# Kernel tuning notes

Measured on AMD Instinct MI355X. Metric: run time of the kernel, lower is better.

The kernel has to match this reference:

```python
import jax, jax.numpy as jnp
import numpy as np

N, E, G = 50000, 500000, 2000   # nodes, edges, graphs
IN, H, ED, OUT = 64, 128, 16, 1
NUM_GAT = 2                      # num_layers - 1
T = 2                            # num_timesteps


def leaky(x, s=0.01):
    return jnp.where(x >= 0, x, s * x)


def gru_cell(x, h, wih, whh, bih, bhh):
    gi = x @ wih.T + bih
    gh = h @ whh.T + bhh
    ir, iz, inn = jnp.split(gi, 3, -1)
    hr, hz, hn = jnp.split(gh, 3, -1)
    r = jax.nn.sigmoid(ir + hr)
    z = jax.nn.sigmoid(iz + hz)
    n = jnp.tanh(inn + r * hn)
    return (1.0 - z) * n + z * h


def lstm_cell(x, h, c, wih, whh, bih, bhh):
    g = x @ wih.T + bih + h @ whh.T + bhh
    i, f, gg, o = jnp.split(g, 4, -1)
    c2 = jax.nn.sigmoid(f) * c + jax.nn.sigmoid(i) * jnp.tanh(gg)
    h2 = jax.nn.sigmoid(o) * jnp.tanh(c2)
    return h2, c2


def setup_inputs() -> dict:
    key = jax.random.key(0)
    ks = iter(jax.random.split(key, 40))
    def rn(shape, s=0.05):
        return jax.random.normal(next(ks), shape, jnp.float32) * s
    return {
        "x": jax.random.normal(next(ks), (N, IN), jnp.float32),
        "edge_index": jax.random.randint(next(ks), (2, E), 0, N),
        "edge_attr": jax.random.normal(next(ks), (E, ED), jnp.float32),
        "batch": jnp.sort(jax.random.randint(next(ks), (N,), 0, G)),
        "lin1_w": rn((H, IN)), "lin1_b": rn((H,)),
        "nd_lin1_w": rn((H, H + ED)), "nd_lin2_w": rn((H, H)), "nd_bias": rn((H,)),
        "gru0_wih": rn((3 * H, H)), "gru0_whh": rn((3 * H, H)),
        "gru0_bih": rn((3 * H,)), "gru0_bhh": rn((3 * H,)),
        "gat_w": rn((NUM_GAT, H, H)), "gat_asrc": rn((NUM_GAT, H)),
        "gat_adst": rn((NUM_GAT, H)), "gat_b": rn((NUM_GAT, H)),
        "gru_wih": rn((NUM_GAT, 3 * H, H)), "gru_whh": rn((NUM_GAT, 3 * H, H)),
        "gru_bih": rn((NUM_GAT, 3 * H)), "gru_bhh": rn((NUM_GAT, 3 * H)),
        "gin_w": rn((H, H)), "gin_b": rn((H,)),
        "lstm_wih": rn((4 * H, H)), "lstm_whh": rn((4 * H, H)),
        "lstm_bih": rn((4 * H,)), "lstm_bhh": rn((4 * H,)),
        "lin2_w": rn((OUT, H)), "lin2_b": rn((OUT,)),
    }


def reference(x, edge_index, edge_attr, batch,
              lin1_w, lin1_b, nd_lin1_w, nd_lin2_w, nd_bias,
              gru0_wih, gru0_whh, gru0_bih, gru0_bhh,
              gat_w, gat_asrc, gat_adst, gat_b,
              gru_wih, gru_whh, gru_bih, gru_bhh,
              gin_w, gin_b, lstm_wih, lstm_whh, lstm_bih, lstm_bhh,
              lin2_w, lin2_b):
    src, dst = edge_index[0], edge_index[1]  # PyG: messages flow src(j) -> dst(i)
    # input projection
    x1 = leaky(x @ lin1_w.T + lin1_b)
    # nd_conv: gather -> MLP -> scatter-add (dropout=0 in eval)
    m = leaky(jnp.concatenate([x1[src], edge_attr], -1) @ nd_lin1_w.T) @ nd_lin2_w.T
    h = jax.nn.elu(jax.ops.segment_sum(m, dst, num_segments=N) + nd_bias)
    xcur = jax.nn.relu(gru_cell(h, x1, gru0_wih, gru0_whh, gru0_bih, gru0_bhh))
    # GAT layers (heads=1, no self loops, negative_slope=0.01)
    for l in range(NUM_GAT):
        xp = xcur @ gat_w[l].T
        a = leaky(xp[src] @ gat_asrc[l] + xp[dst] @ gat_adst[l], 0.01)
        amax = jax.lax.stop_gradient(jax.ops.segment_max(a, dst, num_segments=N))
        ae = jnp.exp(a - amax[dst])
        denom = jax.ops.segment_sum(ae, dst, num_segments=N)
        alpha = ae / denom[dst]
        h = jax.nn.elu(jax.ops.segment_sum(alpha[:, None] * xp[src], dst, num_segments=N) + gat_b[l])
        xcur = jax.nn.relu(gru_cell(h, xcur,
                                    gru_wih[l], gru_whh[l], gru_bih[l], gru_bhh[l]))
    # global readout: GIN on bipartite (nodes -> graphs) + LSTM refinement
    agg = jax.ops.segment_sum(xcur, batch, num_segments=G)  # [G, H], constant over timesteps
    out = jax.nn.relu(agg)
    for _ in range(T):
        h = jax.nn.elu((out + agg) @ gin_w.T + gin_b)  # GIN eps=0: nn(x_dst + aggr)
        out, _ = lstm_cell(out, h, h, lstm_wih, lstm_whh, lstm_bih, lstm_bhh)
    return out @ lin2_w.T + lin2_b  # [G, OUT]
```

## Files before the change

### kernel.cpp

```cpp
#include <hip/hip_runtime.h>
#include <cstdint>
#include <cmath>

#define NN 50000
#define EE 500000
#define GG 2000

#define DEV __device__ __forceinline__

typedef __attribute__((ext_vector_type(8))) short short8;
typedef __attribute__((ext_vector_type(4))) float floatx4;
typedef _Float16 half2v __attribute__((ext_vector_type(2)));
typedef _Float16 half4v __attribute__((ext_vector_type(4)));
typedef _Float16 half8v __attribute__((ext_vector_type(8)));

DEV float fsig(float x) { return 1.f / (1.f + __expf(-x)); }
DEV float ftanh(float x) {
    const float e = __expf(-2.f * fabsf(x));
    const float t = (1.f - e) / (1.f + e);
    return x >= 0.f ? t : -t;
}

DEV float actf(float x, int act) {
    if (act == 1) return x >= 0.f ? x : 0.01f * x;
    if (act == 2) return x > 0.f ? x : __expf(x) - 1.f;
    if (act == 3) return x > 0.f ? x : 0.f;
    return x;
}

DEV float hdot2(half2v a, half2v b, float c) {
#if __has_builtin(__builtin_amdgcn_fdot2)
    return __builtin_amdgcn_fdot2(a, b, c, false);
#else
    return c + (float)a[0] * (float)b[0] + (float)a[1] * (float)b[1];
#endif
}

#define H2(v, i) __builtin_shufflevector(v, v, 2 * (i), 2 * (i) + 1)

__global__ __launch_bounds__(256) void gemm_f16_k(
    const _Float16* __restrict__ A, const _Float16* __restrict__ W,
    const float* __restrict__ bias, _Float16* __restrict__ C,
    int M, int K, int Nout, int act)
{
    __shared__ unsigned short Als[64 * 136];
    __shared__ unsigned short Bls[64 * 136];
    const int tid = threadIdx.x;
    const int bm = blockIdx.y * 64;
    const int bn = blockIdx.x * 64;

    const int ks = (K == 128) ? 7 : 6;
    const int km = K - 1;
    const int nch = (64 * K) >> 3;
    for (int i = tid; i < nch; i += 256) {
        const int e8 = i << 3;
        const int r = e8 >> ks;
        const int c = e8 & km;
        short8 av = {};
        if (bm + r < M) av = *(const short8*)(A + (size_t)(bm + r) * K + c);
        *(short8*)(Als + r * 136 + c) = av;
        *(short8*)(Bls + r * 136 + c) = *(const short8*)(W + (size_t)(bn + r) * K + c);
    }
    __syncthreads();

    const int wave = tid >> 6;
    const int lane = tid & 63;
    const int wr = (wave >> 1) * 32;
    const int wc = (wave & 1) * 32;
    const int l15 = lane & 15;
    const int quad = lane >> 4;

    floatx4 acc00 = {}, acc01 = {}, acc10 = {}, acc11 = {};
    for (int k0 = 0; k0 < K; k0 += 32) {
        const half8v a0 = *(const half8v*)(Als + (wr + l15) * 136 + k0 + quad * 8);
        const half8v a1 = *(const half8v*)(Als + (wr + 16 + l15) * 136 + k0 + quad * 8);
        const half8v b0 = *(const half8v*)(Bls + (wc + l15) * 136 + k0 + quad * 8);
        const half8v b1 = *(const half8v*)(Bls + (wc + 16 + l15) * 136 + k0 + quad * 8);
        acc00 = __builtin_amdgcn_mfma_f32_16x16x32_f16(a0, b0, acc00, 0, 0, 0);
        acc01 = __builtin_amdgcn_mfma_f32_16x16x32_f16(a0, b1, acc01, 0, 0, 0);
        acc10 = __builtin_amdgcn_mfma_f32_16x16x32_f16(a1, b0, acc10, 0, 0, 0);
        acc11 = __builtin_amdgcn_mfma_f32_16x16x32_f16(a1, b1, acc11, 0, 0, 0);
    }

    const floatx4* accs[4] = { &acc00, &acc01, &acc10, &acc11 };
#pragma unroll
    for (int r = 0; r < 2; ++r) {
#pragma unroll
        for (int c = 0; c < 2; ++c) {
            const floatx4 a = *accs[r * 2 + c];
            const int n = bn + wc + c * 16 + l15;
            const float bv = bias ? bias[n] : 0.f;
#pragma unroll
            for (int i = 0; i < 4; ++i) {
                const int m = bm + wr + r * 16 + quad * 4 + i;
                if (m < M) C[(size_t)m * Nout + n] = (_Float16)actf(a[i] + bv, act);
            }
        }
    }
}

__global__ __launch_bounds__(256, 4) void gru_fused4_k(
    const _Float16* __restrict__ xin, const _Float16* __restrict__ hin,
    const _Float16* __restrict__ wih, const _Float16* __restrict__ whh,
    const float* __restrict__ bih, const float* __restrict__ bhh,
    _Float16* __restrict__ xout, int M)
{
    __shared__ unsigned short sX[64 * 136];
    __shared__ unsigned short sH[64 * 136];

    const int tid = threadIdx.x;
    const int bm = blockIdx.x * 64;

    for (int i = tid; i < 1024; i += 256) {
        const int e8 = i << 3;
        const int r = e8 >> 7;
        const int c = e8 & 127;
        const int m = bm + r;
        short8 xv = {}, hv = {};
        if (m < M) {
            xv = *(const short8*)(xin + (size_t)m * 128 + c);
            hv = *(const short8*)(hin + (size_t)m * 128 + c);
        }
        *(short8*)(sX + r * 136 + c) = xv;
        *(short8*)(sH + r * 136 + c) = hv;
    }
    __syncthreads();

    const int wave = tid >> 6;
    const int lane = tid & 63;
    const int l15 = lane & 15;
    const int quad = lane >> 4;
    const int j0 = (blockIdx.y * 4 + wave) * 16;
    const int j = j0 + l15;

    const float br  = bih[j] + bhh[j];
    const float bz  = bih[128 + j] + bhh[128 + j];
    const float bni = bih[256 + j];
    const float bnh = bhh[256 + j];

    floatx4 aR[4] = {}, aZ[4] = {}, aNi[4] = {}, aNh[4] = {};

#pragma unroll
    for (int k = 0; k < 4; ++k) {
        const size_t wrow = (size_t)(j0 + l15) * 128 + k * 32 + quad * 8;
        const half8v wri = *(const half8v*)(wih + wrow);
        const half8v wzi = *(const half8v*)(wih + 128 * 128 + wrow);
        const half8v wni = *(const half8v*)(wih + 2 * 128 * 128 + wrow);
        const half8v wrh = *(const half8v*)(whh + wrow);
        const half8v wzh = *(const half8v*)(whh + 128 * 128 + wrow);
        const half8v wnh = *(const half8v*)(whh + 2 * 128 * 128 + wrow);
#pragma unroll
        for (int rf = 0; rf < 4; ++rf) {
            const half8v ax = *(const half8v*)(sX + (rf * 16 + l15) * 136 + k * 32 + quad * 8);
            const half8v ah = *(const half8v*)(sH + (rf * 16 + l15) * 136 + k * 32 + quad * 8);
            aR[rf]  = __builtin_amdgcn_mfma_f32_16x16x32_f16(ax, wri, aR[rf], 0, 0, 0);
            aR[rf]  = __builtin_amdgcn_mfma_f32_16x16x32_f16(ah, wrh, aR[rf], 0, 0, 0);
            aZ[rf]  = __builtin_amdgcn_mfma_f32_16x16x32_f16(ax, wzi, aZ[rf], 0, 0, 0);
            aZ[rf]  = __builtin_amdgcn_mfma_f32_16x16x32_f16(ah, wzh, aZ[rf], 0, 0, 0);
            aNi[rf] = __builtin_amdgcn_mfma_f32_16x16x32_f16(ax, wni, aNi[rf], 0, 0, 0);
            aNh[rf] = __builtin_amdgcn_mfma_f32_16x16x32_f16(ah, wnh, aNh[rf], 0, 0, 0);
        }
    }

#pragma unroll
    for (int rf = 0; rf < 4; ++rf) {
#pragma unroll
        for (int i = 0; i < 4; ++i) {
            const int m = bm + rf * 16 + quad * 4 + i;
            if (m >= M) continue;
            const float rg = fsig(aR[rf][i] + br);
            const float zg = fsig(aZ[rf][i] + bz);
            const float ng = ftanh(aNi[rf][i] + bni + rg * (aNh[rf][i] + bnh));
            const float hp = (float)((const _Float16*)sH)[(rf * 16 + quad * 4 + i) * 136 + j];
            const float v = (1.f - zg) * ng + zg * hp;
            xout[(size_t)m * 128 + j] = (_Float16)(v > 0.f ? v : 0.f);
        }
    }
}

__global__ void hist_k(const int* __restrict__ ei, int* __restrict__ deg, int E)
{
    int e = blockIdx.x * 256 + threadIdx.x;
    if (e >= E) return;
    atomicAdd(deg + ei[E + e], 1);
}

__global__ __launch_bounds__(1024) void scan_part_k(const int* __restrict__ deg,
                                                    int* __restrict__ bsum, int n)
{
    __shared__ int sh[1024];
    const int t = threadIdx.x;
    const int i = blockIdx.x * 1024 + t;
    sh[t] = (i < n) ? deg[i] : 0;
    __syncthreads();
#pragma unroll
    for (int off = 512; off; off >>= 1) {
        if (t < off) sh[t] += sh[t + off];
        __syncthreads();
    }
    if (t == 0) bsum[blockIdx.x] = sh[0];
}

__global__ void scan_tops_k(const int* __restrict__ bsum, int* __restrict__ boff,
                            int nb, int* __restrict__ rowptr, int n)
{
    if (threadIdx.x != 0 || blockIdx.x != 0) return;
    int run = 0;
    for (int b = 0; b < nb; ++b) { boff[b] = run; run += bsum[b]; }
    rowptr[n] = run;
}

__global__ __launch_bounds__(1024) void scan_final_k(const int* __restrict__ deg,
                                                     const int* __restrict__ boff,
                                                     int* __restrict__ rowptr, int n)
{
    __shared__ int sh[1024];
    const int t = threadIdx.x;
    const int i = blockIdx.x * 1024 + t;
    const int v = (i < n) ? deg[i] : 0;
    sh[t] = v;
    __syncthreads();
#pragma unroll
    for (int off = 1; off < 1024; off <<= 1) {
        int add = (t >= off) ? sh[t - off] : 0;
        __syncthreads();
        sh[t] += add;
        __syncthreads();
    }
    if (i < n) rowptr[i] = boff[blockIdx.x] + sh[t] - v;
}

__global__ void fill_csr_k(const int* __restrict__ ei, const int* __restrict__ rowptr,
                           int* __restrict__ cursor, int* __restrict__ csr_src,
                           int* __restrict__ csr_eid, int E)
{
    int e = blockIdx.x * 256 + threadIdx.x;
    if (e >= E) return;
    int s = ei[e], d = ei[E + e];
    int pos = atomicAdd(cursor + d, 1);
    int slot = rowptr[d] + pos;
    csr_src[slot] = s;
    csr_eid[slot] = e;
}

__global__ void gptr_k(const int* __restrict__ batch, int* __restrict__ gptr,
                       int N, int G)
{
    int n = blockIdx.x * 256 + threadIdx.x;
    if (n >= N) return;
    if (n == 0) {
        for (int g = 0; g <= batch[0]; ++g) gptr[g] = 0;
    } else {
        const int a = batch[n - 1], b = batch[n];
        for (int g = a + 1; g <= b; ++g) gptr[g] = n;
    }
    if (n == N - 1) {
        for (int g = batch[N - 1] + 1; g <= G; ++g) gptr[g] = N;
    }
}

__global__ __launch_bounds__(128) void graph_sum_k(
    const _Float16* __restrict__ xc, const int* __restrict__ gptr,
    _Float16* __restrict__ aggH)
{
    const int g = blockIdx.x;
    const int t = threadIdx.x;
    const int n0 = gptr[g], n1 = gptr[g + 1];
    float acc = 0.f;
    for (int n = n0; n < n1; ++n) acc += (float)xc[(size_t)n * 128 + t];
    aggH[(size_t)g * 128 + t] = (_Float16)acc;
}

struct CvtSeg { const float* src; _Float16* dst; int n; };
struct CvtArgs { CvtSeg s[12]; int count; };

__global__ void cvt_multi_k(CvtArgs a)
{
    const int seg = blockIdx.y;
    if (seg >= a.count) return;
    const CvtSeg cs = a.s[seg];
    for (int i = blockIdx.x * 256 + threadIdx.x; i < cs.n; i += gridDim.x * 256)
        cs.dst[i] = (_Float16)cs.src[i];
}

__global__ void cvt_ndwA_k(const float* __restrict__ ndw, _Float16* __restrict__ outp)
{
    int t = blockIdx.x * 256 + threadIdx.x;
    if (t >= 16384) return;
    int r = t >> 7, c = t & 127;
    outp[r * 128 + c] = (_Float16)ndw[r * 144 + c];
}

__global__ void cvt_ndwB_k(const float* __restrict__ ndw, _Float16* __restrict__ outp)
{
    int t = blockIdx.x * 256 + threadIdx.x;
    if (t >= 2048) return;
    int r = t >> 4, k = t & 15;
    outp[r * 16 + k] = (_Float16)ndw[r * 144 + 128 + k];
}

__global__ __launch_bounds__(128) void nd_gather_k(
    const int* __restrict__ rowptr, const int* __restrict__ csr_src,
    const int* __restrict__ csr_eid, const _Float16* __restrict__ eaH,
    const _Float16* __restrict__ wH, const _Float16* __restrict__ pH,
    _Float16* __restrict__ outp)
{
    const int d = blockIdx.x;
    const int t = threadIdx.x;
    const half8v w0 = *(const half8v*)(wH + t * 16);
    const half8v w1 = *(const half8v*)(wH + t * 16 + 8);

    const int b0 = rowptr[d], b1 = rowptr[d + 1];
    float acc = 0.f;
    int s = 0, e = 0;
    if (b0 < b1) { s = csr_src[b0]; e = csr_eid[b0]; }
    for (int i = b0; i < b1; ++i) {
        const int sn = (i + 1 < b1) ? csr_src[i + 1] : 0;
        const int en = (i + 1 < b1) ? csr_eid[i + 1] : 0;
        const half8v e0 = *(const half8v*)(eaH + (size_t)e * 16);
        const half8v e1 = *(const half8v*)(eaH + (size_t)e * 16 + 8);
        const float pv = (float)pH[(size_t)s * 128 + t];
        float q = 0.f;
        q = hdot2(H2(e0, 0), H2(w0, 0), q);
        q = hdot2(H2(e0, 1), H2(w0, 1), q);
        q = hdot2(H2(e0, 2), H2(w0, 2), q);
        q = hdot2(H2(e0, 3), H2(w0, 3), q);
        q = hdot2(H2(e1, 0), H2(w1, 0), q);
        q = hdot2(H2(e1, 1), H2(w1, 1), q);
        q = hdot2(H2(e1, 2), H2(w1, 2), q);
        q = hdot2(H2(e1, 3), H2(w1, 3), q);
        const float v = pv + q;
        acc += v >= 0.f ? v : 0.01f * v;
        s = sn; e = en;
    }
    outp[(size_t)d * 128 + t] = (_Float16)acc;
}

__global__ void node_dots_k(const _Float16* __restrict__ xp,
                            const float* __restrict__ asrc,
                            const float* __restrict__ adst,
                            float* __restrict__ ssrc, float* __restrict__ sdst)
{
    int n = blockIdx.x, t = threadIdx.x;
    float v = (float)xp[(size_t)n * 128 + t];
    float a = v * asrc[t];
    float b = v * adst[t];
    for (int off = 32; off; off >>= 1) { a += __shfl_down(a, off); b += __shfl_down(b, off); }
    __shared__ float sa[2], sb[2];
    if ((t & 63) == 0) { sa[t >> 6] = a; sb[t >> 6] = b; }
    __syncthreads();
    if (t == 0) { ssrc[n] = sa[0] + sa[1]; sdst[n] = sb[0] + sb[1]; }
}

__global__ __launch_bounds__(128) void gat_gather_k(
    const int* __restrict__ rowptr, const int* __restrict__ csr_src,
    const float* __restrict__ ssrc, const float* __restrict__ sdst,
    const _Float16* __restrict__ xp, const float* __restrict__ bias,
    _Float16* __restrict__ outp)
{
    const int d = blockIdx.x;
    const int t = threadIdx.x;
    __shared__ float red[128];
    __shared__ float lw[128];
    __shared__ int   ls[128];
    __shared__ float racc[4][128];

    const int b0 = rowptr[d], b1 = rowptr[d + 1];
    const int deg = b1 - b0;
    const float sdd = sdst[d];

    const int g  = t >> 5;
    const int fq = t & 31;
    float4 acc = make_float4(0.f, 0.f, 0.f, 0.f);
    float dpart = 0.f;
    for (int base = b0; base < b1; base += 128) {
        const int len = min(128, b1 - base);
        if (t < len) {
            const int s = csr_src[base + t];
            float a = ssrc[s] + sdd;
            a = a >= 0.f ? a : 0.01f * a;
            const float w = __expf(a);
            lw[t] = w;
            ls[t] = s;
            dpart += w;
        }
        __syncthreads();
        for (int j = 0; j < len; j += 4) {
            const int jj = j + g;
            if (jj < len) {
                const float w = lw[jj];
                const half4v hv = *(const half4v*)(xp + (size_t)ls[jj] * 128 + fq * 4);
                acc.x += w * (float)hv[0];
                acc.y += w * (float)hv[1];
                acc.z += w * (float)hv[2];
                acc.w += w * (float)hv[3];
            }
        }
        __syncthreads();
    }

    red[t] = dpart;
    __syncthreads();
#pragma unroll
    for (int off = 64; off; off >>= 1) {
        if (t < off) red[t] += red[t + off];
        __syncthreads();
    }
    const float denom = red[0];

    racc[g][fq * 4 + 0] = acc.x;
    racc[g][fq * 4 + 1] = acc.y;
    racc[g][fq * 4 + 2] = acc.z;
    racc[g][fq * 4 + 3] = acc.w;
    __syncthreads();

    const float s4 = racc[0][t] + racc[1][t] + racc[2][t] + racc[3][t];
    float v = (deg > 0 ? s4 / denom : 0.f) + bias[t];
    outp[(size_t)d * 128 + t] = (_Float16)(v > 0.f ? v : __expf(v) - 1.f);
}

__global__ __launch_bounds__(256) void gin_lstm_k(
    const _Float16* __restrict__ aggH,
    const _Float16* __restrict__ ginw, const float* __restrict__ ginb,
    const _Float16* __restrict__ lwih, const _Float16* __restrict__ lwhh,
    const float* __restrict__ lbih, const float* __restrict__ lbhh,
    const float* __restrict__ l2w, const float* __restrict__ l2b,
    float* __restrict__ y, int G)
{
    __shared__ _Float16 sOa[16 * 136];
    __shared__ _Float16 sOb[16 * 136];
    __shared__ _Float16 sG [16 * 136];
    __shared__ _Float16 sT [16 * 136];
    __shared__ float    sC [16 * 128];

    const int tid = threadIdx.x, wave = tid >> 6, lane = tid & 63;
    const int l15 = lane & 15, quad = lane >> 4;
    const int g0 = blockIdx.x * 16;

    {
        const int r = tid >> 4;
        const int c = (tid & 15) * 8;
        half8v v = {};
        if (g0 + r < G) v = *(const half8v*)(aggH + (size_t)(g0 + r) * 128 + c);
        *(half8v*)(sG + r * 136 + c) = v;
        half8v rv;
#pragma unroll
        for (int i = 0; i < 8; ++i) rv[i] = (float)v[i] > 0.f ? v[i] : (_Float16)0.f;
        *(half8v*)(sOa + r * 136 + c) = rv;
    }
    __syncthreads();

    _Float16* sIn = sOa;
    _Float16* sOut = sOb;
#pragma unroll
    for (int ts = 0; ts < 2; ++ts) {
        for (int ci = 0; ci < 2; ++ci) {
            const int j0 = (wave * 2 + ci) * 16;
            floatx4 acc = {};
#pragma unroll
            for (int k = 0; k < 4; ++k) {
                const half8v b = *(const half8v*)(ginw + (size_t)(j0 + l15) * 128 + k * 32 + quad * 8);
                const half8v a = *(const half8v*)(sIn + l15 * 136 + k * 32 + quad * 8)
                               + *(const half8v*)(sG  + l15 * 136 + k * 32 + quad * 8);
                acc = __builtin_amdgcn_mfma_f32_16x16x32_f16(a, b, acc, 0, 0, 0);
            }
            const int j = j0 + l15;
            const float bg = ginb[j];
#pragma unroll
            for (int i = 0; i < 4; ++i) {
                const int row = quad * 4 + i;
                float v = acc[i] + bg;
                v = v > 0.f ? v : __expf(v) - 1.f;
                sT[row * 136 + j] = (_Float16)v;
                sC[row * 128 + j] = v;
            }
        }
        __syncthreads();

        for (int ci = 0; ci < 2; ++ci) {
            const int j0 = (wave * 2 + ci) * 16;
            floatx4 acc[4] = {};
#pragma unroll
            for (int k = 0; k < 4; ++k) {
                const half8v ao = *(const half8v*)(sIn + l15 * 136 + k * 32 + quad * 8);
                const half8v ah = *(const half8v*)(sT  + l15 * 136 + k * 32 + quad * 8);
#pragma unroll
                for (int gt = 0; gt < 4; ++gt) {
                    const half8v bw = *(const half8v*)(lwih + (size_t)(gt * 128 + j0 + l15) * 128 + k * 32 + quad * 8);
                    const half8v bh = *(const half8v*)(lwhh + (size_t)(gt * 128 + j0 + l15) * 128 + k * 32 + quad * 8);
                    acc[gt] = __builtin_amdgcn_mfma_f32_16x16x32_f16(ao, bw, acc[gt], 0, 0, 0);
                    acc[gt] = __builtin_amdgcn_mfma_f32_16x16x32_f16(ah, bh, acc[gt], 0, 0, 0);
                }
            }
            const int j = j0 + l15;
            const float bi_ = lbih[j]       + lbhh[j];
            const float bf_ = lbih[128 + j] + lbhh[128 + j];
            const float bgg = lbih[256 + j] + lbhh[256 + j];
            const float bo_ = lbih[384 + j] + lbhh[384 + j];
#pragma unroll
            for (int i = 0; i < 4; ++i) {
                const int row = quad * 4 + i;
                const float hg = sC[row * 128 + j];
                const float c2 = fsig(acc[1][i] + bf_) * hg
                               + fsig(acc[0][i] + bi_) * ftanh(acc[2][i] + bgg);
                const float on = fsig(acc[3][i] + bo_) * ftanh(c2);
                sOut[row * 136 + j] = (_Float16)on;
            }
        }
        __syncthreads();
        _Float16* tmp = sIn; sIn = sOut; sOut = tmp;
    }

    if (tid < 64) {
        const int r = tid >> 2;
        const int part = tid & 3;
        float v = 0.f;
        for (int j = part * 32; j < part * 32 + 32; ++j)
            v += (float)sIn[r * 136 + j] * l2w[j];
        v += __shfl_down(v, 2);
        v += __shfl_down(v, 1);
        if (part == 0 && g0 + r < G) y[g0 + r] = v + l2b[0];
    }
}


extern "C" void kernel_launch(void* const* d_in, const int* in_sizes, int n_in,
                              void* d_out, int out_size, void* d_ws, size_t ws_size,
                              hipStream_t stream)
{
    const float* x      = (const float*)d_in[0];
    const int*   ei     = (const int*)  d_in[1];
    const float* ea     = (const float*)d_in[2];
    const int*   batch  = (const int*)  d_in[3];
    const float* lin1_w = (const float*)d_in[4];
    const float* lin1_b = (const float*)d_in[5];
    const float* nd1w   = (const float*)d_in[6];
    const float* nd2w   = (const float*)d_in[7];
    const float* ndb    = (const float*)d_in[8];
    const float* g0wih  = (const float*)d_in[9];
    const float* g0whh  = (const float*)d_in[10];
    const float* g0bih  = (const float*)d_in[11];
    const float* g0bhh  = (const float*)d_in[12];
    const float* gatw   = (const float*)d_in[13];
    const float* gatas  = (const float*)d_in[14];
    const float* gatad  = (const float*)d_in[15];
    const float* gatb   = (const float*)d_in[16];
    const float* gwih   = (const float*)d_in[17];
    const float* gwhh   = (const float*)d_in[18];
    const float* gbih   = (const float*)d_in[19];
    const float* gbhh   = (const float*)d_in[20];
    const float* ginw   = (const float*)d_in[21];
    const float* ginb   = (const float*)d_in[22];
    const float* lwih   = (const float*)d_in[23];
    const float* lwhh   = (const float*)d_in[24];
    const float* lbih   = (const float*)d_in[25];
    const float* lbhh   = (const float*)d_in[26];
    const float* l2w    = (const float*)d_in[27];
    const float* l2b    = (const float*)d_in[28];
    float* outp = (float*)d_out;

    const int N = NN, E = EE, G = GG;

    float* ws = (float*)d_ws;
    size_t off = 0;
    auto alloc = [&](size_t n) {
        float* r = ws + off;
        off += (n + 63) & ~(size_t)63;
        return r;
    };
    _Float16* xH    = (_Float16*)alloc((size_t)N * 32);
    _Float16* x1H   = (_Float16*)alloc((size_t)N * 64);
    _Float16* hbufH = (_Float16*)alloc((size_t)N * 64);
    _Float16* accbH = (_Float16*)alloc((size_t)N * 64);
    _Float16* xcH   = (_Float16*)alloc((size_t)N * 64);
    _Float16* pH    = (_Float16*)alloc((size_t)N * 64);
    _Float16* eaH   = (_Float16*)alloc((size_t)E * 8);
    _Float16* aggH  = (_Float16*)alloc((size_t)G * 64);
    _Float16* lin1_wH = (_Float16*)alloc(4096);
    _Float16* nd1wAH  = (_Float16*)alloc(8192);
    _Float16* ndwBH   = (_Float16*)alloc(1024);
    _Float16* nd2wH   = (_Float16*)alloc(8192);
    _Float16* g0wihH  = (_Float16*)alloc(24576);
    _Float16* g0whhH  = (_Float16*)alloc(24576);
    _Float16* gwihH   = (_Float16*)alloc(49152);
    _Float16* gwhhH   = (_Float16*)alloc(49152);
    _Float16* gatwH   = (_Float16*)alloc(16384);
    _Float16* ginwH   = (_Float16*)alloc(8192);
    _Float16* lwihH   = (_Float16*)alloc(32768);
    _Float16* lwhhH   = (_Float16*)alloc(32768);
    float* ssrc = alloc((size_t)N);
    float* sdst = alloc((size_t)N);
    int* deg     = (int*)alloc((size_t)N);
    int* rowptr  = (int*)alloc((size_t)N + 1);
    int* cursor  = (int*)alloc((size_t)N);
    int* bsum    = (int*)alloc(64);
    int* boff    = (int*)alloc(64);
    int* csr_src = (int*)alloc((size_t)E);
    int* csr_eid = (int*)alloc((size_t)E);
    int* gptr    = (int*)alloc((size_t)G + 1);
    (void)ws_size;

    auto gemmh = [&](const _Float16* A, const _Float16* W, const float* bias,
                     _Float16* C, int M, int K, int Nout, int act) {
        dim3 grid(Nout / 64, (M + 63) / 64);
        gemm_f16_k<<<grid, 256, 0, stream>>>(A, W, bias, C, M, K, Nout, act);
    };
    auto nb = [](int n) { return (n + 255) / 256; };

    auto gru = [&](const _Float16* xin, const _Float16* hin,
                   const _Float16* wih, const _Float16* whh,
                   const float* bih, const float* bhh, _Float16* xout) {
        dim3 grid((N + 63) / 64, 2);
        gru_fused4_k<<<grid, 256, 0, stream>>>(
            xin, hin, wih, whh, bih, bhh, xout, N);
    };

    hipMemsetAsync(deg, 0, (size_t)N * 4, stream);
    hipMemsetAsync(cursor, 0, (size_t)N * 4, stream);
    hist_k<<<nb(E), 256, 0, stream>>>(ei, deg, E);
    const int nblk = (N + 1023) / 1024;
    scan_part_k<<<nblk, 1024, 0, stream>>>(deg, bsum, N);
    scan_tops_k<<<1, 64, 0, stream>>>(bsum, boff, nblk, rowptr, N);
    scan_final_k<<<nblk, 1024, 0, stream>>>(deg, boff, rowptr, N);
    fill_csr_k<<<nb(E), 256, 0, stream>>>(ei, rowptr, cursor, csr_src, csr_eid, E);
    gptr_k<<<nb(N), 256, 0, stream>>>(batch, gptr, N, G);

    CvtArgs ca;
    ca.s[0]  = { ea,     eaH,     E * 16 };
    ca.s[1]  = { x,      xH,      N * 64 };
    ca.s[2]  = { lin1_w, lin1_wH, 8192 };
    ca.s[3]  = { nd2w,   nd2wH,   16384 };
    ca.s[4]  = { g0wih,  g0wihH,  49152 };
    ca.s[5]  = { g0whh,  g0whhH,  49152 };
    ca.s[6]  = { gwih,   gwihH,   98304 };
    ca.s[7]  = { gwhh,   gwhhH,   98304 };
    ca.s[8]  = { gatw,   gatwH,   32768 };
    ca.s[9]  = { ginw,   ginwH,   16384 };
    ca.s[10] = { lwih,   lwihH,   65536 };
    ca.s[11] = { lwhh,   lwhhH,   65536 };
    ca.count = 12;
    cvt_multi_k<<<dim3(2048, 12), 256, 0, stream>>>(ca);
    cvt_ndwA_k<<<64, 256, 0, stream>>>(nd1w, nd1wAH);
    cvt_ndwB_k<<<8, 256, 0, stream>>>(nd1w, ndwBH);

    gemmh(xH, lin1_wH, lin1_b, x1H, N, 64, 128, 1);

    gemmh(x1H, nd1wAH, nullptr, pH, N, 128, 128, 0);
    nd_gather_k<<<N, 128, 0, stream>>>(rowptr, csr_src, csr_eid, eaH, ndwBH, pH, accbH);
    gemmh(accbH, nd2wH, ndb, hbufH, N, 128, 128, 2);

    gru(hbufH, x1H, g0wihH, g0whhH, g0bih, g0bhh, xcH);

    const _Float16* xcur = xcH;
    _Float16* xnext = x1H;
    for (int l = 0; l < 2; ++l) {
        gemmh(xcur, gatwH + (size_t)l * 16384, nullptr, pH, N, 128, 128, 0);
        node_dots_k<<<N, 128, 0, stream>>>(pH, gatas + l * 128, gatad + l * 128, ssrc, sdst);
        gat_gather_k<<<N, 128, 0, stream>>>(rowptr, csr_src, ssrc, sdst, pH,
                                            gatb + l * 128, hbufH);
        gru(hbufH, xcur, gwihH + (size_t)l * 49152, gwhhH + (size_t)l * 49152,
            gbih + l * 384, gbhh + l * 384, xnext);
        const _Float16* t = xcur; xcur = xnext; xnext = (_Float16*)t;
    }

    graph_sum_k<<<G, 128, 0, stream>>>(xcur, gptr, aggH);

    gin_lstm_k<<<(G + 15) / 16, 256, 0, stream>>>(
        aggH, ginwH, ginb, lwihH, lwhhH, lbih, lbhh, l2w, l2b, outp, G);
}
```

Measured before the change: 624.1 us.

## Fuse lin1 with node-update GEMM, fold GAT dots into GEMM, parallelize nd gather

A new kernel computes lin1 and the nd_lin1 projection back to back, keeping the intermediate x1 tile in shared memory. This removes one GEMM launch and the re-read of x1. The GAT projection GEMM now also computes the per-node source and destination attention dot products in its epilogue, using shuffles and atomicAdd into pre-zeroed buffers, which replaces the separate node_dots kernel. nd_gather now splits each node's edges across four thread groups, each handling four features with vector loads, and reduces them through shared memory. This shortens the per-node serial edge chain. In exchange it adds atomics, an extra memset, and results that depend on float atomic ordering.

```diff
diff --git a/kernel.cpp b/kernel.cpp
--- a/kernel.cpp
+++ b/kernel.cpp
@@ -99,6 +99,183 @@
     }
 }
 
+__global__ __launch_bounds__(256) void gemm_dots_k(
+    const _Float16* __restrict__ A, const _Float16* __restrict__ W,
+    _Float16* __restrict__ C, const float* __restrict__ asrc,
+    const float* __restrict__ adst, float* __restrict__ ssrc,
+    float* __restrict__ sdst, int M)
+{
+    __shared__ unsigned short Als[64 * 136];
+    __shared__ unsigned short Bls[64 * 136];
+    const int tid = threadIdx.x;
+    const int bm = blockIdx.y * 64;
+    const int bn = blockIdx.x * 64;
+
+    for (int i = tid; i < 1024; i += 256) {
+        const int e8 = i << 3;
+        const int r = e8 >> 7;
+        const int c = e8 & 127;
+        short8 av = {};
+        if (bm + r < M) av = *(const short8*)(A + (size_t)(bm + r) * 128 + c);
+        *(short8*)(Als + r * 136 + c) = av;
+        *(short8*)(Bls + r * 136 + c) = *(const short8*)(W + (size_t)(bn + r) * 128 + c);
+    }
+    __syncthreads();
+
+    const int wave = tid >> 6;
+    const int lane = tid & 63;
+    const int wr = (wave >> 1) * 32;
+    const int wc = (wave & 1) * 32;
+    const int l15 = lane & 15;
+    const int quad = lane >> 4;
+
+    floatx4 acc00 = {}, acc01 = {}, acc10 = {}, acc11 = {};
+    for (int k0 = 0; k0 < 128; k0 += 32) {
+        const half8v a0 = *(const half8v*)(Als + (wr + l15) * 136 + k0 + quad * 8);
+        const half8v a1 = *(const half8v*)(Als + (wr + 16 + l15) * 136 + k0 + quad * 8);
+        const half8v b0 = *(const half8v*)(Bls + (wc + l15) * 136 + k0 + quad * 8);
+        const half8v b1 = *(const half8v*)(Bls + (wc + 16 + l15) * 136 + k0 + quad * 8);
+        acc00 = __builtin_amdgcn_mfma_f32_16x16x32_f16(a0, b0, acc00, 0, 0, 0);
+        acc01 = __builtin_amdgcn_mfma_f32_16x16x32_f16(a0, b1, acc01, 0, 0, 0);
+        acc10 = __builtin_amdgcn_mfma_f32_16x16x32_f16(a1, b0, acc10, 0, 0, 0);
+        acc11 = __builtin_amdgcn_mfma_f32_16x16x32_f16(a1, b1, acc11, 0, 0, 0);
+    }
+
+    const floatx4* accs[4] = { &acc00, &acc01, &acc10, &acc11 };
+#pragma unroll
+    for (int r = 0; r < 2; ++r)
+#pragma unroll
+        for (int c = 0; c < 2; ++c) {
+            const floatx4 a = *accs[r * 2 + c];
+            const int n = bn + wc + c * 16 + l15;
+#pragma unroll
+            for (int i = 0; i < 4; ++i) {
+                const int m = bm + wr + r * 16 + quad * 4 + i;
+                if (m < M) C[(size_t)m * 128 + n] = (_Float16)a[i];
+            }
+        }
+
+    const int n0 = bn + wc + l15;
+    const int n1 = n0 + 16;
+    const float as0 = asrc[n0], as1 = asrc[n1];
+    const float ad0 = adst[n0], ad1 = adst[n1];
+#pragma unroll
+    for (int r = 0; r < 2; ++r) {
+        const floatx4 a0 = r ? acc10 : acc00;
+        const floatx4 a1 = r ? acc11 : acc01;
+#pragma unroll
+        for (int i = 0; i < 4; ++i) {
+            float vs = a0[i] * as0 + a1[i] * as1;
+            float vd = a0[i] * ad0 + a1[i] * ad1;
+            vs += __shfl_down(vs, 8, 16);
+            vs += __shfl_down(vs, 4, 16);
+            vs += __shfl_down(vs, 2, 16);
+            vs += __shfl_down(vs, 1, 16);
+            vd += __shfl_down(vd, 8, 16);
+            vd += __shfl_down(vd, 4, 16);
+            vd += __shfl_down(vd, 2, 16);
+            vd += __shfl_down(vd, 1, 16);
+            const int m = bm + wr + r * 16 + quad * 4 + i;
+            if (l15 == 0 && m < M) {
+                atomicAdd(ssrc + m, vs);
+                atomicAdd(sdst + m, vd);
+            }
+        }
+    }
+}
+
+__global__ __launch_bounds__(256) void lin1p_k(
+    const _Float16* __restrict__ xH, const _Float16* __restrict__ lin1_wH,
+    const float* __restrict__ lin1_b, const _Float16* __restrict__ nd1wAH,
+    _Float16* __restrict__ x1H, _Float16* __restrict__ pH, int M)
+{
+    __shared__ _Float16 sXin[64 * 72];
+    __shared__ _Float16 sX1 [64 * 136];
+    const int tid = threadIdx.x;
+    const int bm = blockIdx.x * 64;
+
+    for (int i = tid; i < 512; i += 256) {
+        const int e8 = i << 3;
+        const int r = e8 >> 6;
+        const int c = e8 & 63;
+        const int m = bm + r;
+        half8v v = {};
+        if (m < M) v = *(const half8v*)(xH + (size_t)m * 64 + c);
+        *(half8v*)(sXin + r * 72 + c) = v;
+    }
+    __syncthreads();
+
+    const int wave = tid >> 6, lane = tid & 63;
+    const int l15 = lane & 15, quad = lane >> 4;
+    const int wr = (wave >> 1) * 32;
+    const int wc = (wave & 1) * 64;
+
+    {
+        floatx4 acc[2][4] = {};
+#pragma unroll
+        for (int k = 0; k < 2; ++k) {
+            half8v a[2];
+#pragma unroll
+            for (int rf = 0; rf < 2; ++rf)
+                a[rf] = *(const half8v*)(sXin + (wr + rf * 16 + l15) * 72 + k * 32 + quad * 8);
+#pragma unroll
+            for (int ct = 0; ct < 4; ++ct) {
+                const half8v b = *(const half8v*)(lin1_wH + (size_t)(wc + ct * 16 + l15) * 64 + k * 32 + quad * 8);
+#pragma unroll
+                for (int rf = 0; rf < 2; ++rf)
+                    acc[rf][ct] = __builtin_amdgcn_mfma_f32_16x16x32_f16(a[rf], b, acc[rf][ct], 0, 0, 0);
+            }
+        }
+#pragma unroll
+        for (int rf = 0; rf < 2; ++rf)
+#pragma unroll
+            for (int ct = 0; ct < 4; ++ct) {
+                const int n = wc + ct * 16 + l15;
+                const float bv = lin1_b[n];
+#pragma unroll
+                for (int i = 0; i < 4; ++i) {
+                    const int rloc = wr + rf * 16 + quad * 4 + i;
+                    float v = acc[rf][ct][i] + bv;
+                    v = v >= 0.f ? v : 0.01f * v;
+                    const _Float16 h = (_Float16)v;
+                    sX1[rloc * 136 + n] = h;
+                    const int m = bm + rloc;
+                    if (m < M) x1H[(size_t)m * 128 + n] = h;
+                }
+            }
+    }
+    __syncthreads();
+
+    {
+        floatx4 acc[2][4] = {};
+#pragma unroll
+        for (int k = 0; k < 4; ++k) {
+            half8v a[2];
+#pragma unroll
+            for (int rf = 0; rf < 2; ++rf)
+                a[rf] = *(const half8v*)(sX1 + (wr + rf * 16 + l15) * 136 + k * 32 + quad * 8);
+#pragma unroll
+            for (int ct = 0; ct < 4; ++ct) {
+                const half8v b = *(const half8v*)(nd1wAH + (size_t)(wc + ct * 16 + l15) * 128 + k * 32 + quad * 8);
+#pragma unroll
+                for (int rf = 0; rf < 2; ++rf)
+                    acc[rf][ct] = __builtin_amdgcn_mfma_f32_16x16x32_f16(a[rf], b, acc[rf][ct], 0, 0, 0);
+            }
+        }
+#pragma unroll
+        for (int rf = 0; rf < 2; ++rf)
+#pragma unroll
+            for (int ct = 0; ct < 4; ++ct) {
+                const int n = wc + ct * 16 + l15;
+#pragma unroll
+                for (int i = 0; i < 4; ++i) {
+                    const int m = bm + wr + rf * 16 + quad * 4 + i;
+                    if (m < M) pH[(size_t)m * 128 + n] = (_Float16)acc[rf][ct][i];
+                }
+            }
+    }
+}
+
 __global__ __launch_bounds__(256, 4) void gru_fused4_k(
     const _Float16* __restrict__ xin, const _Float16* __restrict__ hin,
     const _Float16* __restrict__ wih, const _Float16* __restrict__ whh,
@@ -305,51 +482,47 @@
     const _Float16* __restrict__ wH, const _Float16* __restrict__ pH,
     _Float16* __restrict__ outp)
 {
+    __shared__ float racc[4][128];
     const int d = blockIdx.x;
     const int t = threadIdx.x;
-    const half8v w0 = *(const half8v*)(wH + t * 16);
-    const half8v w1 = *(const half8v*)(wH + t * 16 + 8);
+    const int g  = t >> 5;
+    const int fq = t & 31;
+
+    half8v w0[4], w1[4];
+#pragma unroll
+    for (int f = 0; f < 4; ++f) {
+        w0[f] = *(const half8v*)(wH + (fq * 4 + f) * 16);
+        w1[f] = *(const half8v*)(wH + (fq * 4 + f) * 16 + 8);
+    }
 
     const int b0 = rowptr[d], b1 = rowptr[d + 1];
-    float acc = 0.f;
-    int s = 0, e = 0;
-    if (b0 < b1) { s = csr_src[b0]; e = csr_eid[b0]; }
-    for (int i = b0; i < b1; ++i) {
-        const int sn = (i + 1 < b1) ? csr_src[i + 1] : 0;
-        const int en = (i + 1 < b1) ? csr_eid[i + 1] : 0;
+    float acc[4] = {};
+    for (int i = b0 + g; i < b1; i += 4) {
+        const int s = csr_src[i], e = csr_eid[i];
         const half8v e0 = *(const half8v*)(eaH + (size_t)e * 16);
         const half8v e1 = *(const half8v*)(eaH + (size_t)e * 16 + 8);
-        const float pv = (float)pH[(size_t)s * 128 + t];
-        float q = 0.f;
-        q = hdot2(H2(e0, 0), H2(w0, 0), q);
-        q = hdot2(H2(e0, 1), H2(w0, 1), q);
-        q = hdot2(H2(e0, 2), H2(w0, 2), q);
-        q = hdot2(H2(e0, 3), H2(w0, 3), q);
-        q = hdot2(H2(e1, 0), H2(w1, 0), q);
-        q = hdot2(H2(e1, 1), H2(w1, 1), q);
-        q = hdot2(H2(e1, 2), H2(w1, 2), q);
-        q = hdot2(H2(e1, 3), H2(w1, 3), q);
-        const float v = pv + q;
-        acc += v >= 0.f ? v : 0.01f * v;
-        s = sn; e = en;
-    }
-    outp[(size_t)d * 128 + t] = (_Float16)acc;
-}
-
-__global__ void node_dots_k(const _Float16* __restrict__ xp,
-                            const float* __restrict__ asrc,
-                            const float* __restrict__ adst,
-                            float* __restrict__ ssrc, float* __restrict__ sdst)
-{
-    int n = blockIdx.x, t = threadIdx.x;
-    float v = (float)xp[(size_t)n * 128 + t];
-    float a = v * asrc[t];
-    float b = v * adst[t];
-    for (int off = 32; off; off >>= 1) { a += __shfl_down(a, off); b += __shfl_down(b, off); }
-    __shared__ float sa[2], sb[2];
-    if ((t & 63) == 0) { sa[t >> 6] = a; sb[t >> 6] = b; }
-    __syncthreads();
-    if (t == 0) { ssrc[n] = sa[0] + sa[1]; sdst[n] = sb[0] + sb[1]; }
+        const half4v p4 = *(const half4v*)(pH + (size_t)s * 128 + fq * 4);
+#pragma unroll
+        for (int f = 0; f < 4; ++f) {
+            float q = 0.f;
+            q = hdot2(H2(e0, 0), H2(w0[f], 0), q);
+            q = hdot2(H2(e0, 1), H2(w0[f], 1), q);
+            q = hdot2(H2(e0, 2), H2(w0[f], 2), q);
+            q = hdot2(H2(e0, 3), H2(w0[f], 3), q);
+            q = hdot2(H2(e1, 0), H2(w1[f], 0), q);
+            q = hdot2(H2(e1, 1), H2(w1[f], 1), q);
+            q = hdot2(H2(e1, 2), H2(w1[f], 2), q);
+            q = hdot2(H2(e1, 3), H2(w1[f], 3), q);
+            const float v = (float)p4[f] + q;
+            acc[f] += v >= 0.f ? v : 0.01f * v;
+        }
+    }
+#pragma unroll
+    for (int f = 0; f < 4; ++f) racc[g][fq * 4 + f] = acc[f];
+    __syncthreads();
+
+    outp[(size_t)d * 128 + t] =
+        (_Float16)(racc[0][t] + racc[1][t] + racc[2][t] + racc[3][t]);
 }
 
 __global__ __launch_bounds__(128) void gat_gather_k(
@@ -560,6 +733,7 @@
     float* outp = (float*)d_out;
 
     const int N = NN, E = EE, G = GG;
+    const int Npad = (N + 63) & ~63;
 
     float* ws = (float*)d_ws;
     size_t off = 0;
@@ -588,8 +762,10 @@
     _Float16* ginwH   = (_Float16*)alloc(8192);
     _Float16* lwihH   = (_Float16*)alloc(32768);
     _Float16* lwhhH   = (_Float16*)alloc(32768);
-    float* ssrc = alloc((size_t)N);
-    float* sdst = alloc((size_t)N);
+    float* ssrcA = alloc((size_t)N);
+    float* sdstA = alloc((size_t)N);
+    float* ssrcB = alloc((size_t)N);
+    float* sdstB = alloc((size_t)N);
     int* deg     = (int*)alloc((size_t)N);
     int* rowptr  = (int*)alloc((size_t)N + 1);
     int* cursor  = (int*)alloc((size_t)N);
@@ -617,6 +793,7 @@
 
     hipMemsetAsync(deg, 0, (size_t)N * 4, stream);
     hipMemsetAsync(cursor, 0, (size_t)N * 4, stream);
+    hipMemsetAsync(ssrcA, 0, (size_t)Npad * 4 * 4, stream);
     hist_k<<<nb(E), 256, 0, stream>>>(ei, deg, E);
     const int nblk = (N + 1023) / 1024;
     scan_part_k<<<nblk, 1024, 0, stream>>>(deg, bsum, N);
@@ -643,9 +820,9 @@
     cvt_ndwA_k<<<64, 256, 0, stream>>>(nd1w, nd1wAH);
     cvt_ndwB_k<<<8, 256, 0, stream>>>(nd1w, ndwBH);
 
-    gemmh(xH, lin1_wH, lin1_b, x1H, N, 64, 128, 1);
-
-    gemmh(x1H, nd1wAH, nullptr, pH, N, 128, 128, 0);
+    lin1p_k<<<(N + 63) / 64, 256, 0, stream>>>(
+        xH, lin1_wH, lin1_b, nd1wAH, x1H, pH, N);
+
     nd_gather_k<<<N, 128, 0, stream>>>(rowptr, csr_src, csr_eid, eaH, ndwBH, pH, accbH);
     gemmh(accbH, nd2wH, ndb, hbufH, N, 128, 128, 2);
 
@@ -654,9 +831,13 @@
     const _Float16* xcur = xcH;
     _Float16* xnext = x1H;
     for (int l = 0; l < 2; ++l) {
-        gemmh(xcur, gatwH + (size_t)l * 16384, nullptr, pH, N, 128, 128, 0);
-        node_dots_k<<<N, 128, 0, stream>>>(pH, gatas + l * 128, gatad + l * 128, ssrc, sdst);
-        gat_gather_k<<<N, 128, 0, stream>>>(rowptr, csr_src, ssrc, sdst, pH,
+        float* ss = l ? ssrcB : ssrcA;
+        float* sd = l ? sdstB : sdstA;
+        dim3 grid(2, (N + 63) / 64);
+        gemm_dots_k<<<grid, 256, 0, stream>>>(
+            xcur, gatwH + (size_t)l * 16384, pH,
+            gatas + l * 128, gatad + l * 128, ss, sd, N);
+        gat_gather_k<<<N, 128, 0, stream>>>(rowptr, csr_src, ss, sd, pH,
                                             gatb + l * 128, hbufH);
         gru(hbufH, xcur, gwihH + (size_t)l * 49152, gwhhH + (size_t)l * 49152,
             gbih + l * 384, gbhh + l * 384, xnext);
```

Result: slower. 639.8 us (+2.5%).
